# Kernel tuning notes

Hardware: AMD Instinct MI355X
Metric: run time of the kernel (lower is better)

Reference implementation:

```python
import jax, jax.numpy as jnp
import numpy as np

VERTICES = 100000
N_CLUSTERS = 25000
BATCH = 1024


def setup_inputs() -> dict:
    key = jax.random.key(0)
    k1, k2 = jax.random.split(key)
    # input features per cluster: [batch, n_clusters]
    x = jax.random.normal(k1, (BATCH, N_CLUSTERS), dtype=jnp.float32)
    # vertex -> cluster map (inverse of the coarsening list-of-lists);
    # pool_matrix[i, j] = 1  iff  v2c[i] == j
    v2c = jax.random.randint(k2, (VERTICES,), 0, N_CLUSTERS, dtype=jnp.int32)
    return {"x": x, "v2c": v2c}


def reference(x, v2c):
    # F.linear(x, pool_matrix) with a 0/1 one-hot-row pool_matrix is exactly a
    # gather: out[..., v] = x[..., v2c[v]]  -> [batch, vertices]
    return jnp.take(x, v2c, axis=-1)
```

## Files before the change

### kernel.cpp

```cpp
#include <hip/hip_runtime.h>

#define VERTS   100000
#define NCLUST  25000
#define BATCH_N 1024
#define THREADS 1024

typedef float  f32x4 __attribute__((ext_vector_type(4)));
typedef int    i32x4 __attribute__((ext_vector_type(4)));

__global__ __launch_bounds__(THREADS) void gather_lds_kernel(
    const float* __restrict__ x,
    const int*   __restrict__ v2c,
    float*       __restrict__ out)
{
    extern __shared__ float lds[];
    const int b   = blockIdx.x;
    const int tid = threadIdx.x;

    const f32x4* __restrict__ xrow4 =
        reinterpret_cast<const f32x4*>(x + (size_t)b * NCLUST);
    f32x4* lds4 = reinterpret_cast<f32x4*>(lds);
    for (int i = tid; i < NCLUST / 4; i += THREADS) {
        lds4[i] = __builtin_nontemporal_load(&xrow4[i]);
    }
    __syncthreads();

    const i32x4* __restrict__ v2c4 = reinterpret_cast<const i32x4*>(v2c);
    f32x4* __restrict__ out4 =
        reinterpret_cast<f32x4*>(out + (size_t)b * VERTS);
    for (int q = tid; q < VERTS / 4; q += THREADS) {
        const i32x4 idx = v2c4[q];
        f32x4 o;
        o.x = lds[idx.x];
        o.y = lds[idx.y];
        o.z = lds[idx.z];
        o.w = lds[idx.w];
        __builtin_nontemporal_store(o, &out4[q]);
    }
}

extern "C" void kernel_launch(void* const* d_in, const int* in_sizes, int n_in,
                              void* d_out, int out_size, void* d_ws, size_t ws_size,
                              hipStream_t stream) {
    const float* x   = (const float*)d_in[0];
    const int*   v2c = (const int*)d_in[1];
    float*       out = (float*)d_out;

    const int lds_bytes = NCLUST * (int)sizeof(float);
    static bool attr_set = false;
    if (!attr_set) {
        hipFuncSetAttribute(reinterpret_cast<const void*>(gather_lds_kernel),
                            hipFuncAttributeMaxDynamicSharedMemorySize, lds_bytes);
        attr_set = true;
    }

    gather_lds_kernel<<<BATCH_N, THREADS, lds_bytes, stream>>>(x, v2c, out);
}
```

Baseline: 480.6 us.

## Pipeline next-row prefetch into registers while gathering current row from LDS

Each block now handles four batch rows instead of one. While it gathers the current row from LDS, it prefetches the next row's x into registers, then copies those registers into LDS after a sync. v2c indices are also software-prefetched one chunk ahead. The aim is to hide global load latency behind the LDS gather and stores. In exchange the grid shrinks to 256 blocks on a GPU with many CUs, so occupancy and load balance drop, and register pressure rises.

```diff
diff --git a/kernel.cpp b/kernel.cpp
--- a/kernel.cpp
+++ b/kernel.cpp
@@ -1,41 +1,106 @@
 #include <hip/hip_runtime.h>
 
-#define VERTS   100000
-#define NCLUST  25000
-#define BATCH_N 1024
-#define THREADS 1024
+#define VERTS    100000
+#define NCLUST   25000
+#define BATCH_N  1024
+#define THREADS  1024
+#define RPB      4
+#define NBLOCKS  (BATCH_N / RPB)
+#define NC4      (NCLUST / 4)
+#define NV4      (VERTS / 4)
+#define NSTG     7
+#define NCHUNK   6
+#define TAILQ    (NV4 - NCHUNK * 4 * THREADS)
 
 typedef float  f32x4 __attribute__((ext_vector_type(4)));
 typedef int    i32x4 __attribute__((ext_vector_type(4)));
 
-__global__ __launch_bounds__(THREADS) void gather_lds_kernel(
+__global__ __launch_bounds__(THREADS) void gather_pipe_kernel(
     const float* __restrict__ x,
     const int*   __restrict__ v2c,
     float*       __restrict__ out)
 {
     extern __shared__ float lds[];
-    const int b   = blockIdx.x;
-    const int tid = threadIdx.x;
-
-    const f32x4* __restrict__ xrow4 =
-        reinterpret_cast<const f32x4*>(x + (size_t)b * NCLUST);
-    f32x4* lds4 = reinterpret_cast<f32x4*>(lds);
-    for (int i = tid; i < NCLUST / 4; i += THREADS) {
-        lds4[i] = __builtin_nontemporal_load(&xrow4[i]);
-    }
-    __syncthreads();
+    const int tid  = threadIdx.x;
+    const int row0 = blockIdx.x * RPB;
 
     const i32x4* __restrict__ v2c4 = reinterpret_cast<const i32x4*>(v2c);
-    f32x4* __restrict__ out4 =
-        reinterpret_cast<f32x4*>(out + (size_t)b * VERTS);
-    for (int q = tid; q < VERTS / 4; q += THREADS) {
-        const i32x4 idx = v2c4[q];
-        f32x4 o;
-        o.x = lds[idx.x];
-        o.y = lds[idx.y];
-        o.z = lds[idx.z];
-        o.w = lds[idx.w];
-        __builtin_nontemporal_store(o, &out4[q]);
+
+    f32x4 stage[NSTG];
+    {
+        const f32x4* __restrict__ xr =
+            reinterpret_cast<const f32x4*>(x + (size_t)row0 * NCLUST);
+        #pragma unroll
+        for (int k = 0; k < NSTG; ++k) {
+            const int i = tid + k * THREADS;
+            if (k < NSTG - 1 || i < NC4)
+                stage[k] = __builtin_nontemporal_load(&xr[i]);
+        }
+    }
+
+    for (int r = 0; r < RPB; ++r) {
+        f32x4* lds4 = reinterpret_cast<f32x4*>(lds);
+        #pragma unroll
+        for (int k = 0; k < NSTG; ++k) {
+            const int i = tid + k * THREADS;
+            if (k < NSTG - 1 || i < NC4) lds4[i] = stage[k];
+        }
+        __syncthreads();
+
+        const bool more = (r + 1 < RPB);
+        const int rn = more ? (row0 + r + 1) : row0;
+        const f32x4* __restrict__ xn =
+            reinterpret_cast<const f32x4*>(x + (size_t)rn * NCLUST);
+        f32x4* __restrict__ out4 = reinterpret_cast<f32x4*>(
+            out + (size_t)(row0 + r) * VERTS);
+
+        i32x4 id[4];
+        #pragma unroll
+        for (int k = 0; k < 4; ++k) id[k] = v2c4[tid + k * THREADS];
+
+        #pragma unroll
+        for (int c = 0; c < NCHUNK; ++c) {
+            i32x4 idn[4];
+            if (c + 1 < NCHUNK) {
+                #pragma unroll
+                for (int k = 0; k < 4; ++k)
+                    idn[k] = v2c4[tid + ((c + 1) * 4 + k) * THREADS];
+            }
+            if (more) {
+                if (c < NSTG - 1)
+                    stage[c] = __builtin_nontemporal_load(&xn[tid + c * THREADS]);
+                if (c == NCHUNK - 1) {
+                    const int i = tid + (NSTG - 1) * THREADS;
+                    if (i < NC4)
+                        stage[NSTG - 1] = __builtin_nontemporal_load(&xn[i]);
+                }
+            }
+            #pragma unroll
+            for (int k = 0; k < 4; ++k) {
+                const i32x4 ix = id[k];
+                f32x4 o;
+                o.x = lds[ix.x];
+                o.y = lds[ix.y];
+                o.z = lds[ix.z];
+                o.w = lds[ix.w];
+                __builtin_nontemporal_store(o, &out4[tid + (c * 4 + k) * THREADS]);
+            }
+            if (c + 1 < NCHUNK) {
+                #pragma unroll
+                for (int k = 0; k < 4; ++k) id[k] = idn[k];
+            }
+        }
+        if (tid < TAILQ) {
+            const int q = tid + NCHUNK * 4 * THREADS;
+            const i32x4 ix = v2c4[q];
+            f32x4 o;
+            o.x = lds[ix.x];
+            o.y = lds[ix.y];
+            o.z = lds[ix.z];
+            o.w = lds[ix.w];
+            __builtin_nontemporal_store(o, &out4[q]);
+        }
+        __syncthreads();
     }
 }
 
@@ -49,10 +114,10 @@
     const int lds_bytes = NCLUST * (int)sizeof(float);
     static bool attr_set = false;
     if (!attr_set) {
-        hipFuncSetAttribute(reinterpret_cast<const void*>(gather_lds_kernel),
+        hipFuncSetAttribute(reinterpret_cast<const void*>(gather_pipe_kernel),
                             hipFuncAttributeMaxDynamicSharedMemorySize, lds_bytes);
         attr_set = true;
     }
 
-    gather_lds_kernel<<<BATCH_N, THREADS, lds_bytes, stream>>>(x, v2c, out);
+    gather_pipe_kernel<<<NBLOCKS, THREADS, lds_bytes, stream>>>(x, v2c, out);
 }
```

New measurement: 484.2 us. About the same (+0.8%).
